# Kernel optimization log

Measured on AMD Instinct MI355X. Metric: run time of the kernel, lower is better.

The kernel has to match this reference:

```python
import jax, jax.numpy as jnp
import numpy as np

N = 100000
E = 2000000
F = 64          # in_features == out_features (required by attention * h_j)
BETA = 0.5
NEG_SLOPE = 0.01  # torch F.leaky_relu default


def setup_inputs() -> dict:
    key = jax.random.key(0)
    k1, k2, k3, k4, k5, k6 = jax.random.split(key, 6)
    h = jax.random.normal(k1, (N, F), dtype=jnp.float32)
    adj = jax.random.randint(k2, (2, E), 0, N, dtype=jnp.int64)
    amount = jax.random.uniform(k3, (E,), dtype=jnp.float32)
    count = jax.random.uniform(k4, (E,), dtype=jnp.float32)
    fc_w = jax.random.normal(k5, (F, 2 * F), dtype=jnp.float32) * (1.0 / np.sqrt(2 * F))
    fc_b = jax.random.normal(k6, (F,), dtype=jnp.float32) * 0.01
    return {"h": h, "adj": adj, "amount": amount, "count": count,
            "fc_w": fc_w, "fc_b": fc_b}


def _minmax_norm(x):
    lo, hi = x.min(), x.max()
    return (x - lo) / (hi - lo + 1e-8)


def reference(h, adj, amount, count, fc_w, fc_b):
    # per-edge weight from normalized amount/count
    edge_weight = BETA * _minmax_norm(amount) + (1.0 - BETA) * _minmax_norm(count)  # [E]

    src, dst = adj[0], adj[1]
    h_i = h[src]                     # [E, F]
    h_j = h[dst]                     # [E, F]
    h_cat = jnp.concatenate([h_i, h_j], axis=1)  # [E, 2F]

    score = jnp.einsum('ef,of->eo', h_cat, fc_w) + fc_b  # [E, F_out]
    score = jnp.where(score >= 0, score, NEG_SLOPE * score)  # leaky_relu
    score = score * edge_weight[:, None]

    # softmax over ALL edges (dim 0), per feature, as in the original
    attention = jax.nn.softmax(score, axis=0)  # [E, F]

    agg = jnp.zeros_like(h).at[src].add(attention * h_j)  # scatter-add -> [N, F]
    return agg
```

## Files before the change

kernel.cpp:

```cpp
#include <hip/hip_runtime.h>
#include <hip/hip_fp16.h>
#include <math.h>

#define FDIM   64
#define NB     64
#define BSHIFT 7
#define BMASK  127
#define CHUNKA 4096
#define CHUNKM 2048
#define CAP    3072
#define CAPB   3584

__global__ __launch_bounds__(256) void mm_k(const float* __restrict__ amount,
                                            const float* __restrict__ count,
                                            float4* __restrict__ partial, int E) {
  __shared__ float4 lred[4];
  float amin = 3.4e38f, amax = -3.4e38f, cmin = 3.4e38f, cmax = -3.4e38f;
  int e0 = blockIdx.x * CHUNKM + threadIdx.x * 8;
  if (e0 + 8 <= E) {
    #pragma unroll
    for (int q = 0; q < 8; q += 4) {
      float4 a4 = *(const float4*)(amount + e0 + q);
      float4 c4 = *(const float4*)(count + e0 + q);
      amin = fminf(amin, fminf(fminf(a4.x, a4.y), fminf(a4.z, a4.w)));
      amax = fmaxf(amax, fmaxf(fmaxf(a4.x, a4.y), fmaxf(a4.z, a4.w)));
      cmin = fminf(cmin, fminf(fminf(c4.x, c4.y), fminf(c4.z, c4.w)));
      cmax = fmaxf(cmax, fmaxf(fmaxf(c4.x, c4.y), fmaxf(c4.z, c4.w)));
    }
  } else {
    for (int e = e0; e < E; e++) {
      float a = amount[e], c = count[e];
      amin = fminf(amin, a); amax = fmaxf(amax, a);
      cmin = fminf(cmin, c); cmax = fmaxf(cmax, c);
    }
  }
  #pragma unroll
  for (int off = 32; off; off >>= 1) {
    amin = fminf(amin, __shfl_down(amin, off));
    amax = fmaxf(amax, __shfl_down(amax, off));
    cmin = fminf(cmin, __shfl_down(cmin, off));
    cmax = fmaxf(cmax, __shfl_down(cmax, off));
  }
  if ((threadIdx.x & 63) == 0) lred[threadIdx.x >> 6] = make_float4(amin, amax, cmin, cmax);
  __syncthreads();
  if (threadIdx.x == 0) {
    float4 r = lred[0];
    #pragma unroll
    for (int w = 1; w < 4; w++) {
      r.x = fminf(r.x, lred[w].x); r.y = fmaxf(r.y, lred[w].y);
      r.z = fminf(r.z, lred[w].z); r.w = fmaxf(r.w, lred[w].w);
    }
    partial[blockIdx.x] = r;
  }
}

__global__ __launch_bounds__(256) void init_k(const float4* __restrict__ partial,
                                              int nb, float* __restrict__ mmf,
                                              int* __restrict__ cursor, int nbkt,
                                              double* __restrict__ colsum) {
  int t = threadIdx.x;
  for (int k = t; k < nbkt; k += 256) cursor[k] = k * CAPB;
  for (int i = t; i < 1024; i += 256) colsum[i] = 0.0;
  float amin = 3.4e38f, amax = -3.4e38f, cmin = 3.4e38f, cmax = -3.4e38f;
  for (int i = t; i < nb; i += 256) {
    float4 p = partial[i];
    amin = fminf(amin, p.x); amax = fmaxf(amax, p.y);
    cmin = fminf(cmin, p.z); cmax = fmaxf(cmax, p.w);
  }
  #pragma unroll
  for (int off = 32; off; off >>= 1) {
    amin = fminf(amin, __shfl_down(amin, off));
    amax = fmaxf(amax, __shfl_down(amax, off));
    cmin = fminf(cmin, __shfl_down(cmin, off));
    cmax = fmaxf(cmax, __shfl_down(cmax, off));
  }
  __shared__ float4 lred[4];
  if ((t & 63) == 0) lred[t >> 6] = make_float4(amin, amax, cmin, cmax);
  __syncthreads();
  if (t == 0) {
    float4 r = lred[0];
    #pragma unroll
    for (int w = 1; w < 4; w++) {
      r.x = fminf(r.x, lred[w].x); r.y = fmaxf(r.y, lred[w].y);
      r.z = fminf(r.z, lred[w].z); r.w = fmaxf(r.w, lred[w].w);
    }
    mmf[0] = r.x; mmf[1] = r.y; mmf[2] = r.z; mmf[3] = r.w;
  }
}

__global__ __launch_bounds__(256) void scatter_k(const int* __restrict__ src,
                                                 const int* __restrict__ dst,
                                                 const float* __restrict__ amount,
                                                 const float* __restrict__ count,
                                                 const float* __restrict__ mmf,
                                                 int* __restrict__ cursor,
                                                 int2* __restrict__ payload,
                                                 int E, int nbkt) {
  __shared__ int cntb[1024];
  __shared__ int baseb[1024];
  __shared__ int sbase[1024];
  __shared__ int wsum[4];
  __shared__ int2 lpay[CHUNKA];
  __shared__ unsigned short lbkt[CHUNKA];
  const int t = threadIdx.x, blk = blockIdx.x;
  for (int k = t; k < nbkt; k += 256) cntb[k] = 0;
  __syncthreads();
  const float amin = mmf[0], amax = mmf[1], cmin = mmf[2], cmax = mmf[3];
  const float L2E = 1.4426950408889634f;
  const float ascale = 0.5f * L2E / (amax - amin + 1e-8f);
  const float cscale = 0.5f * L2E / (cmax - cmin + 1e-8f);
  int e0 = blk * CHUNKA + t * 16;
  const bool full = (e0 + 16 <= E);
  int4 S[4]; int4 D[4]; float4 A[4]; float4 C[4];
  if (full) {
    #pragma unroll
    for (int q = 0; q < 4; q++) {
      S[q] = *(const int4*)(src + e0 + 4 * q);
      D[q] = *(const int4*)(dst + e0 + 4 * q);
      A[q] = *(const float4*)(amount + e0 + 4 * q);
      C[q] = *(const float4*)(count + e0 + 4 * q);
      atomicAdd(&cntb[S[q].x >> BSHIFT], 1);
      atomicAdd(&cntb[S[q].y >> BSHIFT], 1);
      atomicAdd(&cntb[S[q].z >> BSHIFT], 1);
      atomicAdd(&cntb[S[q].w >> BSHIFT], 1);
    }
  } else {
    for (int e = e0; e < E; e++) atomicAdd(&cntb[src[e] >> BSHIFT], 1);
  }
  __syncthreads();
  {
    const int wv = t >> 6, ln = t & 63;
    int carry = 0;
    #pragma unroll
    for (int c = 0; c < 4; c++) {
      int idx = (wv << 8) + (c << 6) + ln;
      int x = (idx < nbkt) ? cntb[idx] : 0;
      int v = x;
      #pragma unroll
      for (int off = 1; off < 64; off <<= 1) {
        int u = __shfl_up(v, off);
        if (ln >= off) v += u;
      }
      if (idx < nbkt) baseb[idx] = carry + v - x;
      carry += __shfl(v, 63);
    }
    if (ln == 0) wsum[wv] = carry;
  }
  __syncthreads();
  {
    const int wv = t >> 6, ln = t & 63;
    int wpre = 0;
    #pragma unroll
    for (int i = 0; i < 4; i++) wpre += (i < wv) ? wsum[i] : 0;
    if (wpre) {
      #pragma unroll
      for (int c = 0; c < 4; c++) {
        int idx = (wv << 8) + (c << 6) + ln;
        if (idx < nbkt) baseb[idx] += wpre;
      }
    }
  }
  __syncthreads();
  for (int k = t; k < nbkt; k += 256) {
    int cnt = cntb[k];
    if (cnt) sbase[k] = atomicAdd(&cursor[k], cnt);
    cntb[k] = baseb[k];
  }
  __syncthreads();
  auto ins = [&](int s, int d, float a, float c) {
    int b = s >> BSHIFT;
    float ew = (a - amin) * ascale + (c - cmin) * cscale;
    int pos = atomicAdd(&cntb[b], 1);
    lpay[pos] = make_int2((d << 8) | (s & BMASK), __float_as_int(ew));
    lbkt[pos] = (unsigned short)b;
  };
  if (full) {
    #pragma unroll
    for (int q = 0; q < 4; q++) {
      ins(S[q].x, D[q].x, A[q].x, C[q].x);
      ins(S[q].y, D[q].y, A[q].y, C[q].y);
      ins(S[q].z, D[q].z, A[q].z, C[q].z);
      ins(S[q].w, D[q].w, A[q].w, C[q].w);
    }
  } else {
    for (int e = e0; e < E; e++) ins(src[e], dst[e], amount[e], count[e]);
  }
  __syncthreads();
  const int ned = min(CHUNKA, E - blk * CHUNKA);
  for (int i = t; i < ned; i += 256) {
    int bk = lbkt[i];
    int gpos = sbase[bk] + (i - baseb[bk]);
    if (gpos < (bk + 1) * CAPB)
      payload[gpos] = lpay[i];
  }
}

__global__ __launch_bounds__(128) void pre_gemm(const float* __restrict__ h,
                                                const float* __restrict__ fc_w,
                                                const float* __restrict__ fc_b,
                                                float* __restrict__ G1,
                                                __half2* __restrict__ P, int N) {
  __shared__ float hs[NB * FDIM];
  const int t = threadIdx.x;
  const int o = t & 63, half = t >> 6;
  float w[FDIM];
  const float* wrow = fc_w + o * 128 + half * 64;
  #pragma unroll
  for (int f = 0; f < FDIM; f += 4) {
    float4 v = *(const float4*)(wrow + f);
    w[f] = v.x; w[f + 1] = v.y; w[f + 2] = v.z; w[f + 3] = v.w;
  }
  const float bias = (half == 0) ? fc_b[o] : 0.0f;
  const int n0 = blockIdx.x * NB;
  const int nrows = min(NB, N - n0);
  for (int i = t; i < nrows * FDIM; i += 128) hs[i] = h[(size_t)n0 * FDIM + i];
  __syncthreads();
  for (int n = 0; n < nrows; n++) {
    float4 a4 = make_float4(0.f, 0.f, 0.f, 0.f);
    #pragma unroll
    for (int f = 0; f < FDIM; f += 4) {
      float4 hv = *(const float4*)(&hs[n * FDIM + f]);
      a4.x += hv.x * w[f];
      a4.y += hv.y * w[f + 1];
      a4.z += hv.z * w[f + 2];
      a4.w += hv.w * w[f + 3];
    }
    float acc = (a4.x + a4.y) + (a4.z + a4.w) + bias;
    if (half == 0) {
      G1[(size_t)(n0 + n) * FDIM + o] = acc;
    } else {
      P[(size_t)(n0 + n) * FDIM + o] =
          __halves2half2(__float2half(acc), __float2half(hs[n * FDIM + o]));
    }
  }
}

__device__ __forceinline__ float2 unpack_h2(unsigned u) {
  __half2 v = *(__half2*)&u;
  return make_float2(__low2float(v), __high2float(v));
}

__global__ __launch_bounds__(512) void fusedB_k(const int2* __restrict__ payload,
                                                const int* __restrict__ cursor,
                                                const float* __restrict__ G1,
                                                const unsigned* __restrict__ P,
                                                double* __restrict__ colsum,
                                                float* __restrict__ out,
                                                int E, int nbkt) {
  __shared__ int2 lpay[CAP];
  __shared__ int fcnt[128];
  __shared__ int fcur[128];
  __shared__ float part[512];
  const int b = blockIdx.x;
  const int t = threadIdx.x;
  const int lane = t & 63;
  const int wv = __builtin_amdgcn_readfirstlane(t >> 6);
  const int node0 = b << BSHIFT;
  const int base = b * CAPB;
  int end = cursor[b];
  if (end > base + CAPB) end = base + CAPB;
  const int nchunks = (end - base + CAP - 1) / CAP;
  const bool multi = (nchunks > 1);
  float csum = 0.0f;
  for (int c = 0; c < nchunks; c++) {
    const int cs = base + c * CAP;
    const int m = min(CAP, end - cs);
    if (t < 128) fcnt[t] = 0;
    __syncthreads();
    int2 myp0, myp1, myp2, myp3, myp4, myp5;
    {
      int i;
      i = t;        if (i < m) { myp0 = payload[cs + i]; atomicAdd(&fcnt[myp0.x & 127], 1); }
      i = t + 512;  if (i < m) { myp1 = payload[cs + i]; atomicAdd(&fcnt[myp1.x & 127], 1); }
      i = t + 1024; if (i < m) { myp2 = payload[cs + i]; atomicAdd(&fcnt[myp2.x & 127], 1); }
      i = t + 1536; if (i < m) { myp3 = payload[cs + i]; atomicAdd(&fcnt[myp3.x & 127], 1); }
      i = t + 2048; if (i < m) { myp4 = payload[cs + i]; atomicAdd(&fcnt[myp4.x & 127], 1); }
      i = t + 2560; if (i < m) { myp5 = payload[cs + i]; atomicAdd(&fcnt[myp5.x & 127], 1); }
    }
    __syncthreads();
    if (wv == 0) {
      int carry = 0;
      #pragma unroll
      for (int cc = 0; cc < 2; cc++) {
        int idx = (cc << 6) + lane;
        int x = fcnt[idx];
        int v = x;
        #pragma unroll
        for (int off = 1; off < 64; off <<= 1) {
          int u = __shfl_up(v, off);
          if (lane >= off) v += u;
        }
        fcur[idx] = carry + v - x;
        carry += __shfl(v, 63);
      }
    }
    __syncthreads();
    {
      int i;
      i = t;        if (i < m) lpay[atomicAdd(&fcur[myp0.x & 127], 1)] = myp0;
      i = t + 512;  if (i < m) lpay[atomicAdd(&fcur[myp1.x & 127], 1)] = myp1;
      i = t + 1024; if (i < m) lpay[atomicAdd(&fcur[myp2.x & 127], 1)] = myp2;
      i = t + 1536; if (i < m) lpay[atomicAdd(&fcur[myp3.x & 127], 1)] = myp3;
      i = t + 2048; if (i < m) lpay[atomicAdd(&fcur[myp4.x & 127], 1)] = myp4;
      i = t + 2560; if (i < m) lpay[atomicAdd(&fcur[myp5.x & 127], 1)] = myp5;
    }
    __syncthreads();
    const int per = (((m + 7) >> 3) + 63) & ~63;
    const int ws = wv * per;
    const int we = min(ws + per, m);
    int curnode = -1;
    bool firstf = true;
    float acc = 0.0f, g1 = 0.0f;
    auto flush_to = [&](int node) {
      if (curnode >= 0) {
        float* dp = out + (size_t)curnode * FDIM + lane;
        if (multi || firstf) { atomicAdd(dp, acc); firstf = false; }
        else *dp = acc;
      }
      curnode = node; acc = 0.0f;
      g1 = G1[(size_t)node * FDIM + lane];
    };
    for (int c0 = ws; c0 < we; c0 += 64) {
      const int mm = min(64, we - c0);
      int2 p = make_int2(0, 0);
      if (lane < mm) p = lpay[c0 + lane];
      if (mm == 64) {
        #pragma unroll 1
        for (int j = 0; j < 64; j += 16) {
          int xs[16]; float ee[16]; unsigned uu[16];
          #pragma unroll
          for (int k = 0; k < 16; k++) {
            xs[k] = __builtin_amdgcn_readlane(p.x, j + k);
            ee[k] = __int_as_float(__builtin_amdgcn_readlane(p.y, j + k));
          }
          #pragma unroll
          for (int k = 0; k < 16; k++) {
            unsigned off = (((unsigned)xs[k]) & 0xFFFFFF00u) | ((unsigned)lane << 2);
            uu[k] = *(const unsigned*)((const char*)P + off);
          }
          #pragma unroll
          for (int k = 0; k < 16; k++) {
            int node = node0 + (xs[k] & 127);
            if (node != curnode) flush_to(node);
            float2 v = unpack_h2(uu[k]);
            float sc = g1 + v.x;
            sc = fmaxf(sc, 0.01f * sc);
            float x = exp2f(sc * ee[k]);
            csum += x;
            acc += x * v.y;
          }
        }
      } else {
        for (int j = 0; j < mm; j += 16) {
          const int rem = mm - j;
          int xs[16]; float ee[16]; unsigned uu[16];
          #pragma unroll
          for (int k = 0; k < 16; k++) {
            xs[k] = __builtin_amdgcn_readlane(p.x, j + k);
            ee[k] = __int_as_float(__builtin_amdgcn_readlane(p.y, j + k));
          }
          #pragma unroll
          for (int k = 0; k < 16; k++) {
            unsigned off = (((unsigned)xs[k]) & 0xFFFFFF00u) | ((unsigned)lane << 2);
            uu[k] = *(const unsigned*)((const char*)P + off);
          }
          #pragma unroll
          for (int k = 0; k < 16; k++) {
            if (k < rem) {
              int node = node0 + (xs[k] & 127);
              if (node != curnode) flush_to(node);
              float2 v = unpack_h2(uu[k]);
              float sc = g1 + v.x;
              sc = fmaxf(sc, 0.01f * sc);
              float x = exp2f(sc * ee[k]);
              csum += x;
              acc += x * v.y;
            }
          }
        }
      }
    }
    if (curnode >= 0) atomicAdd(out + (size_t)curnode * FDIM + lane, acc);
    __syncthreads();
  }
  part[t] = csum;
  __syncthreads();
  if (t < 64) {
    float tot = 0.0f;
    #pragma unroll
    for (int w = 0; w < 8; w++) tot += part[t + (w << 6)];
    atomicAdd(&colsum[t * 16], (double)tot);
  }
}

__global__ __launch_bounds__(256) void scale_k(float4* __restrict__ out4,
                                               const double* __restrict__ colsum,
                                               int total4) {
  __shared__ float rinv_s[64];
  if (threadIdx.x < 64) rinv_s[threadIdx.x] = (float)(1.0 / colsum[threadIdx.x * 16]);
  __syncthreads();
  const float4* r4 = (const float4*)rinv_s;
  int idx = blockIdx.x * blockDim.x + threadIdx.x;
  int stride = gridDim.x * blockDim.x;
  for (int i = idx; i < total4; i += stride) {
    float4 v = out4[i];
    float4 r = r4[i & 15];
    v.x *= r.x; v.y *= r.y; v.z *= r.z; v.w *= r.w;
    out4[i] = v;
  }
}

extern "C" void kernel_launch(void* const* d_in, const int* in_sizes, int n_in,
                              void* d_out, int out_size, void* d_ws, size_t ws_size,
                              hipStream_t stream) {
  const float* h      = (const float*)d_in[0];
  const int*   adj    = (const int*)d_in[1];
  const float* amount = (const float*)d_in[2];
  const float* count  = (const float*)d_in[3];
  const float* fc_w   = (const float*)d_in[4];
  const float* fc_b   = (const float*)d_in[5];
  float* out = (float*)d_out;

  const int E = in_sizes[2];
  const int N = in_sizes[0] / FDIM;
  const int* src = adj;
  const int* dst = adj + E;
  const int nbkt  = (N + BMASK) >> BSHIFT;
  const int nblkA = (E + CHUNKA - 1) / CHUNKA;
  const int nblkM = (E + CHUNKM - 1) / CHUNKM;

  char* ws = (char*)d_ws;
  size_t off = 0;
  auto alloc = [&](size_t bytes) { void* p = ws + off; off += (bytes + 255) & ~(size_t)255; return p; };
  float*    G1      = (float*)alloc((size_t)N * FDIM * sizeof(float));
  __half2*  P       = (__half2*)alloc((size_t)N * FDIM * sizeof(__half2));
  int2*     payload = (int2*)alloc((size_t)nbkt * CAPB * sizeof(int2));
  int*      cursor  = (int*)alloc(1024 * sizeof(int));
  float4*   mmpart  = (float4*)alloc((size_t)nblkM * sizeof(float4));
  double*   colsum  = (double*)alloc(1024 * sizeof(double));
  float*    mmf     = (float*)alloc(4 * sizeof(float));

  mm_k<<<nblkM, 256, 0, stream>>>(amount, count, mmpart, E);
  init_k<<<1, 256, 0, stream>>>(mmpart, nblkM, mmf, cursor, nbkt, colsum);
  scatter_k<<<nblkA, 256, 0, stream>>>(src, dst, amount, count, mmf, cursor, payload, E, nbkt);
  pre_gemm<<<(N + NB - 1) / NB, 128, 0, stream>>>(h, fc_w, fc_b, G1, P, N);
  fusedB_k<<<nbkt, 512, 0, stream>>>(payload, cursor, G1, (const unsigned*)P, colsum, out, E, nbkt);
  scale_k<<<1024, 256, 0, stream>>>((float4*)out, colsum, N * FDIM / 4);
}
```

Baseline: 278.2 us.

## Merge edge bucketing and node pre-GEMM into one launch with block-role dispatch

Combines the scatter (edge bucketing) kernel and the per-node pre-GEMM kernel into a single launch. Block IDs below nblkA do the bucketing and the remaining blocks compute G1/P. The two kernels share LDS through a union, and the GEMM blocks now use 256 threads split across two row halves. This removes a kernel boundary and lets the two independent stages overlap on the GPU. In exchange, every block reserves the larger scatter LDS footprint, which can reduce occupancy for the GEMM blocks.

```diff
diff --git a/kernel.cpp b/kernel.cpp
--- a/kernel.cpp
+++ b/kernel.cpp
@@ -88,149 +88,162 @@
   }
 }
 
-__global__ __launch_bounds__(256) void scatter_k(const int* __restrict__ src,
-                                                 const int* __restrict__ dst,
-                                                 const float* __restrict__ amount,
-                                                 const float* __restrict__ count,
-                                                 const float* __restrict__ mmf,
-                                                 int* __restrict__ cursor,
-                                                 int2* __restrict__ payload,
-                                                 int E, int nbkt) {
-  __shared__ int cntb[1024];
-  __shared__ int baseb[1024];
-  __shared__ int sbase[1024];
-  __shared__ int wsum[4];
-  __shared__ int2 lpay[CHUNKA];
-  __shared__ unsigned short lbkt[CHUNKA];
-  const int t = threadIdx.x, blk = blockIdx.x;
-  for (int k = t; k < nbkt; k += 256) cntb[k] = 0;
-  __syncthreads();
-  const float amin = mmf[0], amax = mmf[1], cmin = mmf[2], cmax = mmf[3];
-  const float L2E = 1.4426950408889634f;
-  const float ascale = 0.5f * L2E / (amax - amin + 1e-8f);
-  const float cscale = 0.5f * L2E / (cmax - cmin + 1e-8f);
-  int e0 = blk * CHUNKA + t * 16;
-  const bool full = (e0 + 16 <= E);
-  int4 S[4]; int4 D[4]; float4 A[4]; float4 C[4];
-  if (full) {
-    #pragma unroll
-    for (int q = 0; q < 4; q++) {
-      S[q] = *(const int4*)(src + e0 + 4 * q);
-      D[q] = *(const int4*)(dst + e0 + 4 * q);
-      A[q] = *(const float4*)(amount + e0 + 4 * q);
-      C[q] = *(const float4*)(count + e0 + 4 * q);
-      atomicAdd(&cntb[S[q].x >> BSHIFT], 1);
-      atomicAdd(&cntb[S[q].y >> BSHIFT], 1);
-      atomicAdd(&cntb[S[q].z >> BSHIFT], 1);
-      atomicAdd(&cntb[S[q].w >> BSHIFT], 1);
-    }
-  } else {
-    for (int e = e0; e < E; e++) atomicAdd(&cntb[src[e] >> BSHIFT], 1);
-  }
-  __syncthreads();
-  {
-    const int wv = t >> 6, ln = t & 63;
-    int carry = 0;
-    #pragma unroll
-    for (int c = 0; c < 4; c++) {
-      int idx = (wv << 8) + (c << 6) + ln;
-      int x = (idx < nbkt) ? cntb[idx] : 0;
-      int v = x;
-      #pragma unroll
-      for (int off = 1; off < 64; off <<= 1) {
-        int u = __shfl_up(v, off);
-        if (ln >= off) v += u;
-      }
-      if (idx < nbkt) baseb[idx] = carry + v - x;
-      carry += __shfl(v, 63);
-    }
-    if (ln == 0) wsum[wv] = carry;
-  }
-  __syncthreads();
-  {
-    const int wv = t >> 6, ln = t & 63;
-    int wpre = 0;
-    #pragma unroll
-    for (int i = 0; i < 4; i++) wpre += (i < wv) ? wsum[i] : 0;
-    if (wpre) {
+union SPMem {
+  struct {
+    int cntb[1024];
+    int baseb[1024];
+    int sbase[1024];
+    int wsum[4];
+    int2 lpay[CHUNKA];
+    unsigned short lbkt[CHUNKA];
+  } sc;
+  float hs[NB * FDIM];
+};
+
+__global__ __launch_bounds__(256) void sp_k(const int* __restrict__ src,
+                                            const int* __restrict__ dst,
+                                            const float* __restrict__ amount,
+                                            const float* __restrict__ count,
+                                            const float* __restrict__ mmf,
+                                            int* __restrict__ cursor,
+                                            int2* __restrict__ payload,
+                                            const float* __restrict__ h,
+                                            const float* __restrict__ fc_w,
+                                            const float* __restrict__ fc_b,
+                                            float* __restrict__ G1,
+                                            __half2* __restrict__ P,
+                                            int E, int nbkt, int nblkA, int N) {
+  __shared__ SPMem sm;
+  const int t = threadIdx.x;
+  if (blockIdx.x < nblkA) {
+    const int blk = blockIdx.x;
+    for (int k = t; k < nbkt; k += 256) sm.sc.cntb[k] = 0;
+    __syncthreads();
+    const float amin = mmf[0], amax = mmf[1], cmin = mmf[2], cmax = mmf[3];
+    const float L2E = 1.4426950408889634f;
+    const float ascale = 0.5f * L2E / (amax - amin + 1e-8f);
+    const float cscale = 0.5f * L2E / (cmax - cmin + 1e-8f);
+    int e0 = blk * CHUNKA + t * 16;
+    const bool full = (e0 + 16 <= E);
+    int4 S[4]; int4 D[4]; float4 A[4]; float4 C[4];
+    if (full) {
+      #pragma unroll
+      for (int q = 0; q < 4; q++) {
+        S[q] = *(const int4*)(src + e0 + 4 * q);
+        D[q] = *(const int4*)(dst + e0 + 4 * q);
+        A[q] = *(const float4*)(amount + e0 + 4 * q);
+        C[q] = *(const float4*)(count + e0 + 4 * q);
+        atomicAdd(&sm.sc.cntb[S[q].x >> BSHIFT], 1);
+        atomicAdd(&sm.sc.cntb[S[q].y >> BSHIFT], 1);
+        atomicAdd(&sm.sc.cntb[S[q].z >> BSHIFT], 1);
+        atomicAdd(&sm.sc.cntb[S[q].w >> BSHIFT], 1);
+      }
+    } else {
+      for (int e = e0; e < E; e++) atomicAdd(&sm.sc.cntb[src[e] >> BSHIFT], 1);
+    }
+    __syncthreads();
+    {
+      const int wv = t >> 6, ln = t & 63;
+      int carry = 0;
       #pragma unroll
       for (int c = 0; c < 4; c++) {
         int idx = (wv << 8) + (c << 6) + ln;
-        if (idx < nbkt) baseb[idx] += wpre;
-      }
-    }
-  }
-  __syncthreads();
-  for (int k = t; k < nbkt; k += 256) {
-    int cnt = cntb[k];
-    if (cnt) sbase[k] = atomicAdd(&cursor[k], cnt);
-    cntb[k] = baseb[k];
-  }
-  __syncthreads();
-  auto ins = [&](int s, int d, float a, float c) {
-    int b = s >> BSHIFT;
-    float ew = (a - amin) * ascale + (c - cmin) * cscale;
-    int pos = atomicAdd(&cntb[b], 1);
-    lpay[pos] = make_int2((d << 8) | (s & BMASK), __float_as_int(ew));
-    lbkt[pos] = (unsigned short)b;
-  };
-  if (full) {
-    #pragma unroll
-    for (int q = 0; q < 4; q++) {
-      ins(S[q].x, D[q].x, A[q].x, C[q].x);
-      ins(S[q].y, D[q].y, A[q].y, C[q].y);
-      ins(S[q].z, D[q].z, A[q].z, C[q].z);
-      ins(S[q].w, D[q].w, A[q].w, C[q].w);
+        int x = (idx < nbkt) ? sm.sc.cntb[idx] : 0;
+        int v = x;
+        #pragma unroll
+        for (int off = 1; off < 64; off <<= 1) {
+          int u = __shfl_up(v, off);
+          if (ln >= off) v += u;
+        }
+        if (idx < nbkt) sm.sc.baseb[idx] = carry + v - x;
+        carry += __shfl(v, 63);
+      }
+      if (ln == 0) sm.sc.wsum[wv] = carry;
+    }
+    __syncthreads();
+    {
+      const int wv = t >> 6, ln = t & 63;
+      int wpre = 0;
+      #pragma unroll
+      for (int i = 0; i < 4; i++) wpre += (i < wv) ? sm.sc.wsum[i] : 0;
+      if (wpre) {
+        #pragma unroll
+        for (int c = 0; c < 4; c++) {
+          int idx = (wv << 8) + (c << 6) + ln;
+          if (idx < nbkt) sm.sc.baseb[idx] += wpre;
+        }
+      }
+    }
+    __syncthreads();
+    for (int k = t; k < nbkt; k += 256) {
+      int cnt = sm.sc.cntb[k];
+      if (cnt) sm.sc.sbase[k] = atomicAdd(&cursor[k], cnt);
+      sm.sc.cntb[k] = sm.sc.baseb[k];
+    }
+    __syncthreads();
+    auto ins = [&](int s, int d, float a, float c) {
+      int b = s >> BSHIFT;
+      float ew = (a - amin) * ascale + (c - cmin) * cscale;
+      int pos = atomicAdd(&sm.sc.cntb[b], 1);
+      sm.sc.lpay[pos] = make_int2((d << 8) | (s & BMASK), __float_as_int(ew));
+      sm.sc.lbkt[pos] = (unsigned short)b;
+    };
+    if (full) {
+      #pragma unroll
+      for (int q = 0; q < 4; q++) {
+        ins(S[q].x, D[q].x, A[q].x, C[q].x);
+        ins(S[q].y, D[q].y, A[q].y, C[q].y);
+        ins(S[q].z, D[q].z, A[q].z, C[q].z);
+        ins(S[q].w, D[q].w, A[q].w, C[q].w);
+      }
+    } else {
+      for (int e = e0; e < E; e++) ins(src[e], dst[e], amount[e], count[e]);
+    }
+    __syncthreads();
+    const int ned = min(CHUNKA, E - blk * CHUNKA);
+    for (int i = t; i < ned; i += 256) {
+      int bk = sm.sc.lbkt[i];
+      int gpos = sm.sc.sbase[bk] + (i - sm.sc.baseb[bk]);
+      if (gpos < (bk + 1) * CAPB)
+        payload[gpos] = sm.sc.lpay[i];
     }
   } else {
-    for (int e = e0; e < E; e++) ins(src[e], dst[e], amount[e], count[e]);
-  }
-  __syncthreads();
-  const int ned = min(CHUNKA, E - blk * CHUNKA);
-  for (int i = t; i < ned; i += 256) {
-    int bk = lbkt[i];
-    int gpos = sbase[bk] + (i - baseb[bk]);
-    if (gpos < (bk + 1) * CAPB)
-      payload[gpos] = lpay[i];
-  }
-}
-
-__global__ __launch_bounds__(128) void pre_gemm(const float* __restrict__ h,
-                                                const float* __restrict__ fc_w,
-                                                const float* __restrict__ fc_b,
-                                                float* __restrict__ G1,
-                                                __half2* __restrict__ P, int N) {
-  __shared__ float hs[NB * FDIM];
-  const int t = threadIdx.x;
-  const int o = t & 63, half = t >> 6;
-  float w[FDIM];
-  const float* wrow = fc_w + o * 128 + half * 64;
-  #pragma unroll
-  for (int f = 0; f < FDIM; f += 4) {
-    float4 v = *(const float4*)(wrow + f);
-    w[f] = v.x; w[f + 1] = v.y; w[f + 2] = v.z; w[f + 3] = v.w;
-  }
-  const float bias = (half == 0) ? fc_b[o] : 0.0f;
-  const int n0 = blockIdx.x * NB;
-  const int nrows = min(NB, N - n0);
-  for (int i = t; i < nrows * FDIM; i += 128) hs[i] = h[(size_t)n0 * FDIM + i];
-  __syncthreads();
-  for (int n = 0; n < nrows; n++) {
-    float4 a4 = make_float4(0.f, 0.f, 0.f, 0.f);
+    const int pgb = blockIdx.x - nblkA;
+    const int o = t & 63;
+    const int grp = t >> 6;
+    const int half = grp & 1;
+    const int rh = grp >> 1;
+    float w[FDIM];
+    const float* wrow = fc_w + o * 128 + half * 64;
     #pragma unroll
     for (int f = 0; f < FDIM; f += 4) {
-      float4 hv = *(const float4*)(&hs[n * FDIM + f]);
-      a4.x += hv.x * w[f];
-      a4.y += hv.y * w[f + 1];
-      a4.z += hv.z * w[f + 2];
-      a4.w += hv.w * w[f + 3];
-    }
-    float acc = (a4.x + a4.y) + (a4.z + a4.w) + bias;
-    if (half == 0) {
-      G1[(size_t)(n0 + n) * FDIM + o] = acc;
-    } else {
-      P[(size_t)(n0 + n) * FDIM + o] =
-          __halves2half2(__float2half(acc), __float2half(hs[n * FDIM + o]));
+      float4 v = *(const float4*)(wrow + f);
+      w[f] = v.x; w[f + 1] = v.y; w[f + 2] = v.z; w[f + 3] = v.w;
+    }
+    const float bias = (half == 0) ? fc_b[o] : 0.0f;
+    const int n0 = pgb * NB;
+    const int nrows = min(NB, N - n0);
+    for (int i = t; i < nrows * FDIM; i += 256) sm.hs[i] = h[(size_t)n0 * FDIM + i];
+    __syncthreads();
+    const int r0 = rh * (NB / 2);
+    const int r1 = min(r0 + NB / 2, nrows);
+    for (int n = r0; n < r1; n++) {
+      float4 a4 = make_float4(0.f, 0.f, 0.f, 0.f);
+      #pragma unroll
+      for (int f = 0; f < FDIM; f += 4) {
+        float4 hv = *(const float4*)(&sm.hs[n * FDIM + f]);
+        a4.x += hv.x * w[f];
+        a4.y += hv.y * w[f + 1];
+        a4.z += hv.z * w[f + 2];
+        a4.w += hv.w * w[f + 3];
+      }
+      float acc = (a4.x + a4.y) + (a4.z + a4.w) + bias;
+      if (half == 0) {
+        G1[(size_t)(n0 + n) * FDIM + o] = acc;
+      } else {
+        P[(size_t)(n0 + n) * FDIM + o] =
+            __halves2half2(__float2half(acc), __float2half(sm.hs[n * FDIM + o]));
+      }
     }
   }
 }
@@ -428,6 +441,7 @@
   const int nbkt  = (N + BMASK) >> BSHIFT;
   const int nblkA = (E + CHUNKA - 1) / CHUNKA;
   const int nblkM = (E + CHUNKM - 1) / CHUNKM;
+  const int npg   = (N + NB - 1) / NB;
 
   char* ws = (char*)d_ws;
   size_t off = 0;
@@ -442,8 +456,8 @@
 
   mm_k<<<nblkM, 256, 0, stream>>>(amount, count, mmpart, E);
   init_k<<<1, 256, 0, stream>>>(mmpart, nblkM, mmf, cursor, nbkt, colsum);
-  scatter_k<<<nblkA, 256, 0, stream>>>(src, dst, amount, count, mmf, cursor, payload, E, nbkt);
-  pre_gemm<<<(N + NB - 1) / NB, 128, 0, stream>>>(h, fc_w, fc_b, G1, P, N);
+  sp_k<<<nblkA + npg, 256, 0, stream>>>(src, dst, amount, count, mmf, cursor, payload,
+                                        h, fc_w, fc_b, G1, P, E, nbkt, nblkA, N);
   fusedB_k<<<nbkt, 512, 0, stream>>>(payload, cursor, G1, (const unsigned*)P, colsum, out, E, nbkt);
   scale_k<<<1024, 256, 0, stream>>>((float4*)out, colsum, N * FDIM / 4);
 }
```

After: 289.9 us. +4.2%, slower.
